# Kernel optimization log

Measured on AMD Instinct MI355X. Metric: run time of the kernel, lower is better.

Reference implementation:

```python
import jax, jax.numpy as jnp
import numpy as np

L, N, E, H = 1024, 8, 1024, 8


def setup_inputs() -> dict:
    key = jax.random.key(0)
    ks = jax.random.split(key, 9)
    s = 0.02
    return {
        "query": jax.random.normal(ks[0], (L, N, E), jnp.float32),
        "key": jax.random.normal(ks[1], (L, N, E), jnp.float32),
        "value": jax.random.normal(ks[2], (L, N, E), jnp.float32),
        "Wqkv": jax.random.normal(ks[3], (H, 3 * E, E), jnp.float32) * s,
        "bqkv": jax.random.normal(ks[4], (H, 3 * E), jnp.float32) * s,
        "Wo": jax.random.normal(ks[5], (H, E, E), jnp.float32) * s,
        "bo": jax.random.normal(ks[6], (H, E), jnp.float32) * s,
        "Wout": jax.random.normal(ks[7], (E, H * E), jnp.float32) * s,
        "bout": jax.random.normal(ks[8], (E,), jnp.float32) * s,
    }


def reference(query, key, value, Wqkv, bqkv, Wo, bo, Wout, bout):
    # Each of H independent single-head MultiheadAttention modules, batched over h.
    Wq, Wk, Wv = Wqkv[:, :E], Wqkv[:, E:2 * E], Wqkv[:, 2 * E:]   # [H,E,E] each
    bq, bk, bv = bqkv[:, :E], bqkv[:, E:2 * E], bqkv[:, 2 * E:]   # [H,E]
    # Projections: (L,N,E) x (H,E,E) -> (H,L,N,E)
    q = jnp.einsum('lne,hde->hlnd', query, Wq) + bq[:, None, None, :]
    k = jnp.einsum('sne,hde->hsnd', key, Wk) + bk[:, None, None, :]
    v = jnp.einsum('sne,hde->hsnd', value, Wv) + bv[:, None, None, :]
    scale = 1.0 / jnp.sqrt(jnp.asarray(E, q.dtype))  # head_dim == E since 1 head per module
    scores = jnp.einsum('hlnd,hsnd->hnls', q, k) * scale  # [H,N,L,S]
    attn_weights = jax.nn.softmax(scores, axis=-1)
    ctx = jnp.einsum('hnls,hsnd->hlnd', attn_weights, v)   # [H,L,N,E]
    head_out = jnp.einsum('hlnd,hed->hlne', ctx, Wo) + bo[:, None, None, :]
    # concat along last dim: (L,N,H*E)
    concat = jnp.transpose(head_out, (1, 2, 0, 3)).reshape(L, N, H * E)
    out = concat @ Wout.T + bout  # (L,N,E)
    return out, attn_weights  # weights: [H,N,L,S] (stack of per-head (N,L,S))
```

## Files before the change

kernel.cpp:

```cpp
#include <hip/hip_runtime.h>
#include <stdint.h>


typedef unsigned short u16;
typedef unsigned int u32;
typedef __attribute__((ext_vector_type(8))) __bf16 bf16x8;
typedef __attribute__((ext_vector_type(4))) float f32x4;
typedef __attribute__((ext_vector_type(4))) u16 u16x4;

#define DEVFN static __device__ __forceinline__

static constexpr int LQ = 1024, NN = 8, EE = 1024, HH = 8, SS = 1024;
static constexpr long LNE = (long)LQ * NN * EE;
static constexpr long MM = 1048576;

static constexpr long OF_QBF   = 0;
static constexpr long OF_KBF   = 8388608;
static constexpr long OF_VALT  = 16777216;
static constexpr long OF_F     = 25165824;
static constexpr long OF_WKT   = 33554432;
static constexpr long OF_WVT   = 41943040;
static constexpr long OF_WOT   = 50331648;
static constexpr long OF_WOUTB = 58720256;
static constexpr long OF_GT    = 67108864;
static constexpr long OF_BM    = 75497472;
static constexpr long OF_T     = 83886080;
static constexpr long OF_P     = 150994944;
static constexpr long OF_SMALL_F = 109051904;

DEVFN u16 f2bf(float x) {
  u32 u = __builtin_bit_cast(u32, x);
  u = (u + 0x7FFFu + ((u >> 16) & 1u)) >> 16;
  return (u16)u;
}
DEVFN float bf2f(u16 x) { return __builtin_bit_cast(float, (u32)x << 16); }

DEVFN void gload16(const u16* g, u16* l) {
  __builtin_amdgcn_global_load_lds(
      (const __attribute__((address_space(1))) void*)(uintptr_t)g,
      (__attribute__((address_space(3))) void*)(uintptr_t)l, 16, 0, 0);
}

#define BAR() asm volatile("s_barrier" ::: "memory")
#define VMCNT2() asm volatile("s_waitcnt vmcnt(2)" ::: "memory")
#define VMCNT0() asm volatile("s_waitcnt vmcnt(0)" ::: "memory")
#define VMCNT8() asm volatile("s_waitcnt vmcnt(8)" ::: "memory")
#define VMCNT10() asm volatile("s_waitcnt vmcnt(10)" ::: "memory")
#define SB0() __builtin_amdgcn_sched_barrier(0)

struct Cvt3P { const float* s[3]; u16* d[3]; };
__global__ __launch_bounds__(256) void k_cvt3(Cvt3P p) {
  const int z = blockIdx.y;
  const float* s = p.s[z];
  u16* d = p.d[z];
  long i = (long)blockIdx.x * 256 + threadIdx.x;
  for (; i < 2097152; i += 131072) {
    float4 v = reinterpret_cast<const float4*>(s)[i];
    u16x4 o;
    o.x = f2bf(v.x); o.y = f2bf(v.y); o.z = f2bf(v.z); o.w = f2bf(v.w);
    reinterpret_cast<u16x4*>(d)[i] = o;
  }
}

struct Tp5P { const float* s[5]; u16* d[5]; int sld[5]; long szs[5]; long dzs[5]; };
__global__ __launch_bounds__(256) void k_tp5(Tp5P p) {
  const int cfg = blockIdx.z >> 3, zz = blockIdx.z & 7;
  const float* src = p.s[cfg] + (long)zz * p.szs[cfg];
  u16* dst = p.d[cfg] + (long)zz * p.dzs[cfg];
  const int sld = p.sld[cfg];
  __shared__ float t[64][65];
  const int r = threadIdx.x >> 4, c4 = (threadIdx.x & 15) * 4;
#pragma unroll
  for (int rr = 0; rr < 64; rr += 16) {
    float4 v = *reinterpret_cast<const float4*>(
        &src[(long)(blockIdx.y * 64 + r + rr) * sld + blockIdx.x * 64 + c4]);
    t[r + rr][c4] = v.x; t[r + rr][c4 + 1] = v.y;
    t[r + rr][c4 + 2] = v.z; t[r + rr][c4 + 3] = v.w;
  }
  __syncthreads();
#pragma unroll
  for (int rr = 0; rr < 64; rr += 16) {
    u16x4 o;
    o.x = f2bf(t[c4][r + rr]);     o.y = f2bf(t[c4 + 1][r + rr]);
    o.z = f2bf(t[c4 + 2][r + rr]); o.w = f2bf(t[c4 + 3][r + rr]);
    *reinterpret_cast<u16x4*>(
        &dst[(long)(blockIdx.x * 64 + r + rr) * 1024 + blockIdx.y * 64 + c4]) = o;
  }
}

__global__ __launch_bounds__(256) void k_bvec(const float* __restrict__ Wqkv,
                                              const float* __restrict__ bqkv,
                                              float* __restrict__ bp) {
  const int ec = blockIdx.x, h = blockIdx.y, dc = blockIdx.z, t = threadIdx.x;
  const int e = ec * 256 + t;
  const float* wk = Wqkv + (long)h * 3145728 + 1048576;
  const float* bq = bqkv + h * 3072;
  float sb = 0.f;
  for (int dd = 0; dd < 128; ++dd) {
    const int d = dc * 128 + dd;
    sb += wk[(long)d * 1024 + e] * bq[d];
  }
  bp[dc * 8192 + h * 1024 + e] = sb;
}
__global__ __launch_bounds__(256) void k_redb(const float* __restrict__ bp,
                                              float* __restrict__ b) {
  const int i = blockIdx.x * 256 + threadIdx.x;
  float sb = 0.f;
#pragma unroll
  for (int dc = 0; dc < 8; ++dc) sb += bp[dc * 8192 + i];
  b[i] = sb;
}

__global__ __launch_bounds__(256) void k_rowdot(const float* __restrict__ X,
                                                const float* __restrict__ V,
                                                float* __restrict__ OUT) {
  const int wave = threadIdx.x >> 6, lane = threadIdx.x & 63;
  const int r = blockIdx.x * 4 + wave;
  const float4* xr = reinterpret_cast<const float4*>(X + (long)r * 1024);
  float acc[8];
#pragma unroll
  for (int h = 0; h < 8; ++h) acc[h] = 0.f;
#pragma unroll
  for (int it = 0; it < 4; ++it) {
    float4 q = xr[it * 64 + lane];
#pragma unroll
    for (int h = 0; h < 8; ++h) {
      float4 av = reinterpret_cast<const float4*>(V + h * 1024)[it * 64 + lane];
      acc[h] += q.x * av.x + q.y * av.y + q.z * av.z + q.w * av.w;
    }
  }
#pragma unroll
  for (int h = 0; h < 8; ++h)
#pragma unroll
    for (int o = 1; o < 64; o <<= 1) acc[h] += __shfl_xor(acc[h], o);
  if (lane == 0) {
    const int idx = r >> 3, n = r & 7;
#pragma unroll
    for (int h = 0; h < 8; ++h) OUT[h * 8192 + n * 1024 + idx] = acc[h];
  }
}

__global__ __launch_bounds__(256) void k_be2(const float* __restrict__ Wout,
                                             const float* __restrict__ bo,
                                             const float* __restrict__ bout,
                                             const float* __restrict__ bqkv,
                                             const u16* __restrict__ Bm,
                                             float* __restrict__ be2) {
  const int e = blockIdx.x, t = threadIdx.x;
  float s = 0.f;
  for (int i = t; i < 8192; i += 256) {
    s += Wout[(long)e * 8192 + i] * bo[i];
    const int h = i >> 10, d = i & 1023;
    s += bf2f(Bm[(long)e * 8192 + i]) * bqkv[h * 3072 + 2048 + d];
  }
#pragma unroll
  for (int o = 1; o < 64; o <<= 1) s += __shfl_xor(s, o);
  __shared__ float ps[4];
  if ((t & 63) == 0) ps[t >> 6] = s;
  __syncthreads();
  if (t == 0) be2[e] = bout[e] + ps[0] + ps[1] + ps[2] + ps[3];
}

__global__ __launch_bounds__(256) void k_combine(const float* __restrict__ p0,
                                                 const float* __restrict__ p1,
                                                 const float* __restrict__ be,
                                                 float* __restrict__ out) {
  long i = (long)blockIdx.x * 256 + threadIdx.x;
  const long st = (long)gridDim.x * 256;
  for (; i < 2097152; i += st) {
    float4 a = reinterpret_cast<const float4*>(p0)[i];
    float4 b = reinterpret_cast<const float4*>(p1)[i];
    float4 c = reinterpret_cast<const float4*>(be)[i & 255];
    float4 o = {a.x + b.x + c.x, a.y + b.y + c.y, a.z + b.z + c.z, a.w + b.w + c.w};
    reinterpret_cast<float4*>(out)[i] = o;
  }
}

struct GemmP {
  const u16* A; const u16* B;
  float* Cf; u16* Cb;
  int lda, ldb, ldc, K, NB;
  long sAh, sAn, sBh, sBn, sCh, sCn;
  float scale;
};
struct GemmP2 { GemmP p0, p1; int split; };

template <int M0, int N0>
DEVFN void quad(f32x4 (&acc)[8][4], bf16x8 (&a)[4][2], bf16x8 (&b)[4][2]) {
#pragma unroll
  for (int mi = 0; mi < 4; ++mi)
#pragma unroll
    for (int ni = 0; ni < 2; ++ni) {
      acc[M0 + mi][N0 + ni] = __builtin_amdgcn_mfma_f32_16x16x32_bf16(
          a[mi][0], b[N0 + ni][0], acc[M0 + mi][N0 + ni], 0, 0, 0);
      acc[M0 + mi][N0 + ni] = __builtin_amdgcn_mfma_f32_16x16x32_bf16(
          a[mi][1], b[N0 + ni][1], acc[M0 + mi][N0 + ni], 0, 0, 0);
    }
}

DEVFN void swz_block(int& bx, int& by, int& bz) {
  long lid = blockIdx.x + (long)gridDim.x * (blockIdx.y + (long)gridDim.y * blockIdx.z);
  const long nwg = (long)gridDim.x * gridDim.y * gridDim.z;
  long s = (nwg % 8 == 0) ? ((lid % 8) * (nwg / 8) + lid / 8) : lid;
  bx = (int)(s % gridDim.x);
  long r2 = s / gridDim.x;
  by = (int)(r2 % gridDim.y);
  bz = (int)(r2 / gridDim.y);
}

template <int OUT_F32>
DEVFN void gemm_body(const GemmP& p, int bx, int by, int bz) {
  const int h = bz / p.NB, n = bz % p.NB;
  const u16* Ab = p.A + (long)h * p.sAh + (long)n * p.sAn;
  const u16* Bb = p.B + (long)h * p.sBh + (long)n * p.sBn;
  const long coff = (long)h * p.sCh + (long)n * p.sCn;
  const int row0 = by * 256;
  const int col0 = bx * 256;

  __shared__ u16 LDSU[65536];

  const int tid = threadIdx.x;
  const int wave = tid >> 6, lane = tid & 63;
  const int wr = wave >> 2, wc = wave & 3;
  const int NT = p.K >> 6;

  f32x4 acc[8][4];
  const f32x4 zero = {0.f, 0.f, 0.f, 0.f};
#pragma unroll
  for (int i = 0; i < 8; ++i)
#pragma unroll
    for (int j = 0; j < 4; ++j) acc[i][j] = zero;

  const int swc = ((lane & 7) ^ ((lane >> 3) & 7)) * 8;
  const u16* Ag = Ab + (long)(row0 + wave * 16 + (lane >> 3)) * p.lda + swc;
  const u16* Bg = Bb + (long)(col0 + wave * 16 + (lane >> 3)) * p.ldb + swc;

  auto STAGE = [&](int hh) {
    const int kt = hh >> 2;
    if (kt < NT) {
      const int pt = hh & 3;
      const int hf = pt >> 1;
      u16* l = &LDSU[((pt & 1) ? 32768 : 0) + (kt & 1) * 16384 + hf * 8192 + wave * 1024];
      const int ld = (pt & 1) ? p.ldb : p.lda;
      const u16* g = ((pt & 1) ? Bg : Ag) + (long)hf * 128 * ld + kt * 64;
      gload16(g, l);
      gload16(g + 8L * ld, l + 512);
    }
  };

  STAGE(0); STAGE(1); STAGE(2); STAGE(3); STAGE(4);
  VMCNT2();
  BAR();

  const int rA = lane & 15;
  const int c0 = (((lane >> 4)) ^ (lane & 7)) * 8;
  const int c1 = ((4 + (lane >> 4)) ^ (lane & 7)) * 8;

  bf16x8 a[4][2], b[4][2];

  for (int t = 0; t < NT; ++t) {
    const int db = (t & 1) * 16384;
    const u16* Ar = &LDSU[db + wr * 8192 + rA * 64];
    const u16* Br = &LDSU[32768 + db + (wc >> 1) * 8192 + ((wc & 1) * 64 + rA) * 64];

#pragma unroll
    for (int mi = 0; mi < 4; ++mi) {
      a[mi][0] = *reinterpret_cast<const bf16x8*>(&Ar[mi * 1024 + c0]);
      a[mi][1] = *reinterpret_cast<const bf16x8*>(&Ar[mi * 1024 + c1]);
    }
#pragma unroll
    for (int ni = 0; ni < 2; ++ni) {
      b[ni][0] = *reinterpret_cast<const bf16x8*>(&Br[ni * 1024 + c0]);
      b[ni][1] = *reinterpret_cast<const bf16x8*>(&Br[ni * 1024 + c1]);
    }
    STAGE(4 * t + 5);
    BAR();
    SB0(); __builtin_amdgcn_s_setprio(1);
    quad<0, 0>(acc, a, b);
    __builtin_amdgcn_s_setprio(0); SB0();
    BAR();

#pragma unroll
    for (int ni = 2; ni < 4; ++ni) {
      b[ni][0] = *reinterpret_cast<const bf16x8*>(&Br[ni * 1024 + c0]);
      b[ni][1] = *reinterpret_cast<const bf16x8*>(&Br[ni * 1024 + c1]);
    }
    STAGE(4 * t + 6);
    BAR();
    SB0(); __builtin_amdgcn_s_setprio(1);
    quad<0, 2>(acc, a, b);
    __builtin_amdgcn_s_setprio(0); SB0();
    BAR();

#pragma unroll
    for (int mi = 0; mi < 4; ++mi) {
      a[mi][0] = *reinterpret_cast<const bf16x8*>(&Ar[(4 + mi) * 1024 + c0]);
      a[mi][1] = *reinterpret_cast<const bf16x8*>(&Ar[(4 + mi) * 1024 + c1]);
    }
    STAGE(4 * t + 7);
    BAR();
    SB0(); __builtin_amdgcn_s_setprio(1);
    quad<4, 0>(acc, a, b);
    __builtin_amdgcn_s_setprio(0); SB0();
    BAR();

    STAGE(4 * t + 8);
    if (t < NT - 2) { VMCNT2(); }
    else if (t == NT - 2) { VMCNT0(); }
    BAR();
    SB0(); __builtin_amdgcn_s_setprio(1);
    quad<4, 2>(acc, a, b);
    __builtin_amdgcn_s_setprio(0); SB0();
    BAR();
  }

  const int crow = (lane >> 4) * 4;
  const int ccol = lane & 15;
#pragma unroll
  for (int mi = 0; mi < 8; ++mi) {
#pragma unroll
    for (int j = 0; j < 4; ++j) {
      const int grow = row0 + wr * 128 + mi * 16 + crow + j;
#pragma unroll
      for (int ni = 0; ni < 4; ++ni) {
        const int gcol = col0 + wc * 64 + ni * 16 + ccol;
        float v = acc[mi][ni][j] * p.scale;
        if constexpr (OUT_F32)
          p.Cf[coff + (long)grow * p.ldc + gcol] = v;
        else
          p.Cb[coff + (long)grow * p.ldc + gcol] = f2bf(v);
      }
    }
  }
}

template <int OUT_F32>
__global__ __launch_bounds__(512, 2) void k_gemm256(GemmP p) {
  int bx, by, bz;
  swz_block(bx, by, bz);
  gemm_body<OUT_F32>(p, bx, by, bz);
}
template <int OUT_F32>
__global__ __launch_bounds__(512, 2) void k_gemm256_pair(GemmP2 pp) {
  int bx, by, bz;
  swz_block(bx, by, bz);
  if (bz < pp.split) gemm_body<OUT_F32>(pp.p0, bx, by, bz);
  else gemm_body<OUT_F32>(pp.p1, bx, by, bz - pp.split);
}

struct FscP {
  const u16* T; const u16* K; const float* beta;
  float* attn; u16* P;
};
__global__ __launch_bounds__(512, 2) void k_fsc(FscP p) {
  const int lid = blockIdx.x + 16 * blockIdx.y;
  const int n = lid & 7;
  const int rest = lid >> 3;
  const int bx = rest & 15;
  const int h = rest >> 4;
  const int row0 = bx * 64;

  __shared__ u16 BT[65536];
  __shared__ u16 AT[8192];
  __shared__ float red[2][64][8];

  const int tid = threadIdx.x;
  const int w = tid >> 6, lane = tid & 63;
  const int rl = lane & 15, g4 = lane >> 4;

  const u16* Abase = p.T + (long)h * 8388608 + n * 1024 + (long)row0 * 8192;
  const int ksw = ((lane & 3) ^ ((lane >> 3) & 3)) * 8;
  const u16* Ag2 = Abase + (long)(lane >> 2) * 8192 + ksw;
  const u16* Bg2 = p.K + n * 1024 + (long)(lane >> 2) * 8192 + ksw;

  f32x4 acc[4][8];
  const f32x4 zero = {0.f, 0.f, 0.f, 0.f};
#pragma unroll
  for (int mi = 0; mi < 4; ++mi)
#pragma unroll
    for (int ni = 0; ni < 8; ++ni) acc[mi][ni] = zero;

  auto STAGE_B = [&](int t) {
    const int bufo = (t & 1) * 32768;
#pragma unroll
    for (int q8 = 0; q8 < 8; ++q8) {
      const int cg = w * 8 + q8;
      gload16(Bg2 + (long)cg * 16 * 8192 + t * 32, &BT[bufo + cg * 512]);
    }
  };
  auto STAGE_A = [&](int t) {
    gload16(Ag2 + (long)w * 16 * 8192 + t * 32, &AT[(t & 3) * 2048 + w * 512]);
  };

  STAGE_B(0); STAGE_B(1);
  if (w < 4) { STAGE_A(0); STAGE_A(1); STAGE_A(2); }
  if (w < 4) { VMCNT10(); } else { VMCNT8(); }
  BAR();

  const int pko = (g4 ^ ((rl >> 1) & 3)) * 8;

  const int NT = 32;
  for (int t = 0; t < NT; ++t) {
    const u16* Ab_ = &AT[(t & 3) * 2048];
    const u16* Bb_ = &BT[(t & 1) * 32768];
    bf16x8 aF[4], bF[8];
#pragma unroll
    for (int mi = 0; mi < 4; ++mi)
      aF[mi] = *reinterpret_cast<const bf16x8*>(&Ab_[(mi * 16 + rl) * 32 + pko]);
#pragma unroll
    for (int ni = 0; ni < 8; ++ni)
      bF[ni] = *reinterpret_cast<const bf16x8*>(
          &Bb_[(w * 128 + ni * 16 + rl) * 32 + pko]);
    SB0(); __builtin_amdgcn_s_setprio(1);
#pragma unroll
    for (int mi = 0; mi < 4; ++mi)
#pragma unroll
      for (int ni = 0; ni < 8; ++ni)
        acc[mi][ni] = __builtin_amdgcn_mfma_f32_16x16x32_bf16(
            aF[mi], bF[ni], acc[mi][ni], 0, 0, 0);
    __builtin_amdgcn_s_setprio(0); SB0();
    BAR();
    if (t + 2 < NT) STAGE_B(t + 2);
    if (w < 4 && t + 3 < NT) STAGE_A(t + 3);
    if (t < NT - 2) {
      if (w < 4) { VMCNT10(); } else { VMCNT8(); }
    } else {
      VMCNT0();
    }
    BAR();
  }

  const float* betap = p.beta + h * 8192 + n * 1024 + w * 128 + rl;
  float betv[8];
#pragma unroll
  for (int ni = 0; ni < 8; ++ni) betv[ni] = betap[ni * 16];

  float rmax[4][4];
#pragma unroll
  for (int mi = 0; mi < 4; ++mi)
#pragma unroll
    for (int j = 0; j < 4; ++j) {
      float m = -3.0e38f;
#pragma unroll
      for (int ni = 0; ni < 8; ++ni) {
        float v = (acc[mi][ni][j] + betv[ni]) * 0.03125f;
        acc[mi][ni][j] = v;
        m = fmaxf(m, v);
      }
      rmax[mi][j] = m;
    }
#pragma unroll
  for (int msk = 1; msk < 16; msk <<= 1)
#pragma unroll
    for (int mi = 0; mi < 4; ++mi)
#pragma unroll
      for (int j = 0; j < 4; ++j)
        rmax[mi][j] = fmaxf(rmax[mi][j], __shfl_xor(rmax[mi][j], msk));
  if (rl == 0) {
#pragma unroll
    for (int mi = 0; mi < 4; ++mi)
#pragma unroll
      for (int j = 0; j < 4; ++j) red[0][mi * 16 + g4 * 4 + j][w] = rmax[mi][j];
  }
  __syncthreads();
  float gmax[4][4];
#pragma unroll
  for (int mi = 0; mi < 4; ++mi)
#pragma unroll
    for (int j = 0; j < 4; ++j) {
      const int row = mi * 16 + g4 * 4 + j;
      float4 x = *reinterpret_cast<const float4*>(&red[0][row][0]);
      float4 y = *reinterpret_cast<const float4*>(&red[0][row][4]);
      gmax[mi][j] = fmaxf(fmaxf(fmaxf(x.x, x.y), fmaxf(x.z, x.w)),
                          fmaxf(fmaxf(y.x, y.y), fmaxf(y.z, y.w)));
    }
  float rsum[4][4];
#pragma unroll
  for (int mi = 0; mi < 4; ++mi)
#pragma unroll
    for (int j = 0; j < 4; ++j) {
      float s = 0.f;
#pragma unroll
      for (int ni = 0; ni < 8; ++ni) {
        float e = __expf(acc[mi][ni][j] - gmax[mi][j]);
        acc[mi][ni][j] = e;
        s += e;
      }
      rsum[mi][j] = s;
    }
#pragma unroll
  for (int msk = 1; msk < 16; msk <<= 1)
#pragma unroll
    for (int mi = 0; mi < 4; ++mi)
#pragma unroll
      for (int j = 0; j < 4; ++j) rsum[mi][j] += __shfl_xor(rsum[mi][j], msk);
  if (rl == 0) {
#pragma unroll
    for (int mi = 0; mi < 4; ++mi)
#pragma unroll
      for (int j = 0; j < 4; ++j) red[1][mi * 16 + g4 * 4 + j][w] = rsum[mi][j];
  }
  __syncthreads();
  float* attn_b = p.attn + ((long)h * 8 + n) * 1048576;
  u16* P_b = p.P + ((long)h * 8 + n) * 1048576;
#pragma unroll
  for (int mi = 0; mi < 4; ++mi)
#pragma unroll
    for (int j = 0; j < 4; ++j) {
      const int row = mi * 16 + g4 * 4 + j;
      float4 x = *reinterpret_cast<const float4*>(&red[1][row][0]);
      float4 y = *reinterpret_cast<const float4*>(&red[1][row][4]);
      const float inv =
          1.0f / (x.x + x.y + x.z + x.w + y.x + y.y + y.z + y.w);
      float* ar = attn_b + (long)(row0 + row) * 1024 + w * 128 + rl;
      u16* pr = P_b + (long)(row0 + row) * 1024 + w * 128 + rl;
#pragma unroll
      for (int ni = 0; ni < 8; ++ni) {
        float v = acc[mi][ni][j] * inv;
        ar[ni * 16] = v;
        pr[ni * 16] = f2bf(v);
      }
    }
}

extern "C" void kernel_launch(void* const* d_in, const int* in_sizes, int n_in,
                              void* d_out, int out_size, void* d_ws,
                              size_t ws_size, hipStream_t stream) {
  const float* query = (const float*)d_in[0];
  const float* key_  = (const float*)d_in[1];
  const float* value = (const float*)d_in[2];
  const float* Wqkv  = (const float*)d_in[3];
  const float* bqkv  = (const float*)d_in[4];
  const float* Wo    = (const float*)d_in[5];
  const float* bo    = (const float*)d_in[6];
  const float* Wout  = (const float*)d_in[7];
  const float* bout  = (const float*)d_in[8];

  float* out  = (float*)d_out;
  float* attn = out + LNE;

  u16* ws = (u16*)d_ws;
  u16* qbf   = ws + OF_QBF;
  u16* kbf   = ws + OF_KBF;
  u16* valT  = ws + OF_VALT;
  u16* WqT_F = ws + OF_F;
  u16* WkT   = ws + OF_WKT;
  u16* WvT   = ws + OF_WVT;
  u16* WoT   = ws + OF_WOT;
  u16* Woutb = ws + OF_WOUTB;
  u16* Gt    = ws + OF_GT;
  u16* Bm    = ws + OF_BM;
  u16* Tbuf  = ws + OF_T;
  u16* Pbuf  = ws + OF_P;
  float* part = (float*)(ws + OF_P);
  float* Sf   = (float*)d_ws + OF_SMALL_F;
  float* beta  = Sf;
  float* bv2   = Sf + 65536;
  float* be2   = Sf + 73728;
  float* bpart = Sf + 74752;

  {
    Cvt3P p;
    p.s[0] = query; p.s[1] = key_; p.s[2] = Wout;
    p.d[0] = qbf;   p.d[1] = kbf;  p.d[2] = Woutb;
    k_cvt3<<<dim3(512, 3), 256, 0, stream>>>(p);
  }
  {
    Tp5P p;
    p.s[0] = Wqkv;           p.d[0] = WqT_F; p.sld[0] = 1024; p.szs[0] = 3145728; p.dzs[0] = MM;
    p.s[1] = Wqkv + 1048576; p.d[1] = WkT;   p.sld[1] = 1024; p.szs[1] = 3145728; p.dzs[1] = MM;
    p.s[2] = Wqkv + 2097152; p.d[2] = WvT;   p.sld[2] = 1024; p.szs[2] = 3145728; p.dzs[2] = MM;
    p.s[3] = Wo;             p.d[3] = WoT;   p.sld[3] = 1024; p.szs[3] = MM;      p.dzs[3] = MM;
    p.s[4] = value;          p.d[4] = valT;  p.sld[4] = 8192; p.szs[4] = 1024;    p.dzs[4] = MM;
    k_tp5<<<dim3(16, 16, 40), 256, 0, stream>>>(p);
  }
  k_bvec<<<dim3(4, 8, 8), 256, 0, stream>>>(Wqkv, bqkv, bpart);
  k_redb<<<32, 256, 0, stream>>>(bpart, bv2);
  k_rowdot<<<2048, 256, 0, stream>>>(key_, bv2, beta);

  const dim3 blk(512);

  {
    GemmP g = {};
    g.A = WkT; g.lda = 1024; g.sAh = MM; g.sAn = 0;
    g.B = WqT_F; g.ldb = 1024; g.sBh = MM; g.sBn = 0;
    g.Cb = Gt; g.ldc = 1024; g.sCh = MM; g.sCn = 0;
    g.K = 1024; g.NB = 1; g.scale = 1.f;
    GemmP m = {};
    m.A = Woutb; m.lda = 8192; m.sAh = 1024; m.sAn = 0;
    m.B = WoT; m.ldb = 1024; m.sBh = MM; m.sBn = 0;
    m.Cb = Bm; m.ldc = 8192; m.sCh = 1024; m.sCn = 0;
    m.K = 1024; m.NB = 1; m.scale = 1.f;
    GemmP2 pp = {g, m, 8};
    k_gemm256_pair<0><<<dim3(4, 4, 16), blk, 0, stream>>>(pp);
  }
  k_be2<<<1024, 256, 0, stream>>>(Wout, bo, bout, bqkv, Bm, be2);
  {
    GemmP t = {};
    t.A = qbf; t.lda = 8192; t.sAh = 0; t.sAn = 1024;
    t.B = Gt; t.ldb = 1024; t.sBh = MM; t.sBn = 0;
    t.Cb = Tbuf; t.ldc = 8192; t.sCh = 8388608; t.sCn = 1024;
    t.K = 1024; t.NB = 8; t.scale = 1.f;
    GemmP f = {};
    f.A = Bm; f.lda = 8192; f.sAh = 1024; f.sAn = 0;
    f.B = WvT; f.ldb = 1024; f.sBh = MM; f.sBn = 0;
    f.Cb = WqT_F; f.ldc = 8192; f.sCh = 1024; f.sCn = 0;
    f.K = 1024; f.NB = 1; f.scale = 1.f;
    GemmP2 pp = {t, f, 64};
    k_gemm256_pair<0><<<dim3(4, 4, 72), blk, 0, stream>>>(pp);
  }
  {
    FscP p = {Tbuf, kbf, beta, attn, Pbuf};
    k_fsc<<<dim3(16, 64), blk, 0, stream>>>(p);
  }
  {
    GemmP p = {};
    p.A = Pbuf; p.lda = 1024; p.sAh = 1048576; p.sAn = 8388608;
    p.B = valT; p.ldb = 1024; p.sBh = 1048576; p.sBn = 0;
    p.Cb = Tbuf; p.ldc = 65536; p.sCh = 8192; p.sCn = 1024;
    p.K = 1024; p.NB = 8; p.scale = 1.f;
    k_gemm256<0><<<dim3(4, 4, 64), blk, 0, stream>>>(p);
  }
  {
    GemmP p = {};
    p.A = Tbuf; p.lda = 8192; p.sAh = 4096; p.sAn = 0;
    p.B = WqT_F; p.ldb = 8192; p.sBh = 4096; p.sBn = 0;
    p.Cf = part; p.ldc = 1024; p.sCh = 8388608; p.sCn = 0;
    p.K = 4096; p.NB = 1; p.scale = 1.f;
    k_gemm256<1><<<dim3(4, 32, 2), blk, 0, stream>>>(p);
  }
  k_combine<<<2048, 256, 0, stream>>>(part, part + 8388608, be2, out);
}
```

Before: 918.9 us.

## Use per-wave private B buffers in score kernel to cut block barriers

Each wave in the fused score/softmax kernel now loads its own 128-column slice of K into a private LDS region, so B-tile reuse no longer needs block-wide barriers. The shared A tile moves to a six-slot ring refilled two k-steps at a time, which drops barriers from two per k-step to one per pair of steps. The reduction scratch now reuses the A buffer, and an extra sync is added between the max and sum reductions. This removes barrier stalls in the main loop, in exchange for more intricate vmcnt accounting and a risk of subtle race bugs.

After: 897.6 us. 1.02x faster.

```diff
diff --git a/kernel.cpp b/kernel.cpp
--- a/kernel.cpp
+++ b/kernel.cpp
@@ -45,7 +45,7 @@
 #define VMCNT2() asm volatile("s_waitcnt vmcnt(2)" ::: "memory")
 #define VMCNT0() asm volatile("s_waitcnt vmcnt(0)" ::: "memory")
 #define VMCNT8() asm volatile("s_waitcnt vmcnt(8)" ::: "memory")
-#define VMCNT10() asm volatile("s_waitcnt vmcnt(10)" ::: "memory")
+#define VMCNT16() asm volatile("s_waitcnt vmcnt(16)" ::: "memory")
 #define SB0() __builtin_amdgcn_sched_barrier(0)
 
 struct Cvt3P { const float* s[3]; u16* d[3]; };
@@ -360,9 +360,8 @@
   const int h = rest >> 4;
   const int row0 = bx * 64;
 
-  __shared__ u16 BT[65536];
-  __shared__ u16 AT[8192];
-  __shared__ float red[2][64][8];
+  __shared__ u16 BW[65536];
+  __shared__ u16 AT[12288];
 
   const int tid = threadIdx.x;
   const int w = tid >> 6, lane = tid & 63;
@@ -371,7 +370,7 @@
   const u16* Abase = p.T + (long)h * 8388608 + n * 1024 + (long)row0 * 8192;
   const int ksw = ((lane & 3) ^ ((lane >> 3) & 3)) * 8;
   const u16* Ag2 = Abase + (long)(lane >> 2) * 8192 + ksw;
-  const u16* Bg2 = p.K + n * 1024 + (long)(lane >> 2) * 8192 + ksw;
+  const u16* Bg2 = p.K + n * 1024 + (long)(w * 128 + (lane >> 2)) * 8192 + ksw;
 
   f32x4 acc[4][8];
   const f32x4 zero = {0.f, 0.f, 0.f, 0.f};
@@ -380,56 +379,59 @@
 #pragma unroll
     for (int ni = 0; ni < 8; ++ni) acc[mi][ni] = zero;
 
+  u16* BWw = &BW[w * 8192];
   auto STAGE_B = [&](int t) {
-    const int bufo = (t & 1) * 32768;
-#pragma unroll
-    for (int q8 = 0; q8 < 8; ++q8) {
-      const int cg = w * 8 + q8;
-      gload16(Bg2 + (long)cg * 16 * 8192 + t * 32, &BT[bufo + cg * 512]);
-    }
+    u16* dst = BWw + (t & 1) * 4096;
+#pragma unroll
+    for (int q8 = 0; q8 < 8; ++q8)
+      gload16(Bg2 + (long)q8 * 16 * 8192 + t * 32, dst + q8 * 512);
   };
-  auto STAGE_A = [&](int t) {
-    gload16(Ag2 + (long)w * 16 * 8192 + t * 32, &AT[(t & 3) * 2048 + w * 512]);
+  auto STAGE_A = [&](int t, int slot) {
+    gload16(Ag2 + (long)w * 16 * 8192 + t * 32, &AT[slot * 2048 + w * 512]);
   };
 
+  if (w < 4) { STAGE_A(0, 0); STAGE_A(1, 1); STAGE_A(2, 2); STAGE_A(3, 3); }
   STAGE_B(0); STAGE_B(1);
-  if (w < 4) { STAGE_A(0); STAGE_A(1); STAGE_A(2); }
-  if (w < 4) { VMCNT10(); } else { VMCNT8(); }
+  VMCNT8();
   BAR();
 
   const int pko = (g4 ^ ((rl >> 1) & 3)) * 8;
 
-  const int NT = 32;
-  for (int t = 0; t < NT; ++t) {
-    const u16* Ab_ = &AT[(t & 3) * 2048];
-    const u16* Bb_ = &BT[(t & 1) * 32768];
-    bf16x8 aF[4], bF[8];
-#pragma unroll
-    for (int mi = 0; mi < 4; ++mi)
-      aF[mi] = *reinterpret_cast<const bf16x8*>(&Ab_[(mi * 16 + rl) * 32 + pko]);
-#pragma unroll
-    for (int ni = 0; ni < 8; ++ni)
-      bF[ni] = *reinterpret_cast<const bf16x8*>(
-          &Bb_[(w * 128 + ni * 16 + rl) * 32 + pko]);
-    SB0(); __builtin_amdgcn_s_setprio(1);
-#pragma unroll
-    for (int mi = 0; mi < 4; ++mi)
+#pragma unroll
+  for (int j = 0; j < 16; ++j) {
+#pragma unroll
+    for (int ti = 0; ti < 2; ++ti) {
+      const int t = 2 * j + ti;
+      const int slot = t % 6;
+      if (t >= 30) { VMCNT0(); } else { VMCNT8(); }
+      const u16* Ab_ = &AT[slot * 2048];
+      const u16* Bb_ = BWw + (t & 1) * 4096;
+      bf16x8 aF[4], bF[8];
+#pragma unroll
+      for (int mi = 0; mi < 4; ++mi)
+        aF[mi] = *reinterpret_cast<const bf16x8*>(&Ab_[(mi * 16 + rl) * 32 + pko]);
 #pragma unroll
       for (int ni = 0; ni < 8; ++ni)
-        acc[mi][ni] = __builtin_amdgcn_mfma_f32_16x16x32_bf16(
-            aF[mi], bF[ni], acc[mi][ni], 0, 0, 0);
-    __builtin_amdgcn_s_setprio(0); SB0();
-    BAR();
-    if (t + 2 < NT) STAGE_B(t + 2);
-    if (w < 4 && t + 3 < NT) STAGE_A(t + 3);
-    if (t < NT - 2) {
-      if (w < 4) { VMCNT10(); } else { VMCNT8(); }
-    } else {
-      VMCNT0();
-    }
-    BAR();
-  }
-
+        bF[ni] = *reinterpret_cast<const bf16x8*>(&Bb_[(ni * 16 + rl) * 32 + pko]);
+      SB0(); __builtin_amdgcn_s_setprio(1);
+#pragma unroll
+      for (int mi = 0; mi < 4; ++mi)
+#pragma unroll
+        for (int ni = 0; ni < 8; ++ni)
+          acc[mi][ni] = __builtin_amdgcn_mfma_f32_16x16x32_bf16(
+              aF[mi], bF[ni], acc[mi][ni], 0, 0, 0);
+      __builtin_amdgcn_s_setprio(0); SB0();
+      if (t + 2 < 32) STAGE_B(t + 2);
+    }
+    if (w < 4 && 2 * j + 4 < 32) {
+      STAGE_A(2 * j + 4, (2 * j + 4) % 6);
+      STAGE_A(2 * j + 5, (2 * j + 5) % 6);
+    }
+    if (w < 4) { VMCNT16(); }
+    BAR();
+  }
+
+  float* RED = reinterpret_cast<float*>(&AT[0]);
   const float* betap = p.beta + h * 8192 + n * 1024 + w * 128 + rl;
   float betv[8];
 #pragma unroll
@@ -460,7 +462,8 @@
 #pragma unroll
     for (int mi = 0; mi < 4; ++mi)
 #pragma unroll
-      for (int j = 0; j < 4; ++j) red[0][mi * 16 + g4 * 4 + j][w] = rmax[mi][j];
+      for (int j = 0; j < 4; ++j)
+        RED[(mi * 16 + g4 * 4 + j) * 8 + w] = rmax[mi][j];
   }
   __syncthreads();
   float gmax[4][4];
@@ -469,8 +472,8 @@
 #pragma unroll
     for (int j = 0; j < 4; ++j) {
       const int row = mi * 16 + g4 * 4 + j;
-      float4 x = *reinterpret_cast<const float4*>(&red[0][row][0]);
-      float4 y = *reinterpret_cast<const float4*>(&red[0][row][4]);
+      float4 x = *reinterpret_cast<const float4*>(&RED[row * 8]);
+      float4 y = *reinterpret_cast<const float4*>(&RED[row * 8 + 4]);
       gmax[mi][j] = fmaxf(fmaxf(fmaxf(x.x, x.y), fmaxf(x.z, x.w)),
                           fmaxf(fmaxf(y.x, y.y), fmaxf(y.z, y.w)));
     }
@@ -494,11 +497,13 @@
     for (int mi = 0; mi < 4; ++mi)
 #pragma unroll
       for (int j = 0; j < 4; ++j) rsum[mi][j] += __shfl_xor(rsum[mi][j], msk);
+  __syncthreads();
   if (rl == 0) {
 #pragma unroll
     for (int mi = 0; mi < 4; ++mi)
 #pragma unroll
-      for (int j = 0; j < 4; ++j) red[1][mi * 16 + g4 * 4 + j][w] = rsum[mi][j];
+      for (int j = 0; j < 4; ++j)
+        RED[512 + (mi * 16 + g4 * 4 + j) * 8 + w] = rsum[mi][j];
   }
   __syncthreads();
   float* attn_b = p.attn + ((long)h * 8 + n) * 1048576;
@@ -508,8 +513,8 @@
 #pragma unroll
     for (int j = 0; j < 4; ++j) {
       const int row = mi * 16 + g4 * 4 + j;
-      float4 x = *reinterpret_cast<const float4*>(&red[1][row][0]);
-      float4 y = *reinterpret_cast<const float4*>(&red[1][row][4]);
+      float4 x = *reinterpret_cast<const float4*>(&RED[512 + row * 8]);
+      float4 y = *reinterpret_cast<const float4*>(&RED[512 + row * 8 + 4]);
       const float inv =
           1.0f / (x.x + x.y + x.z + x.w + y.x + y.y + y.z + y.w);
       float* ar = attn_b + (long)(row0 + row) * 1024 + w * 128 + rl;
```
